# Kernel optimization log

Measured on AMD Instinct MI355X. Metric: run time of the kernel, lower is better.

## Reference

```python
import jax, jax.numpy as jnp
import numpy as np

N_NODES = 50000
N_REL = 256
D_IN = 128
NHID = 128
NHEADS = 2
D_OUT = NHID * NHEADS  # 256
ALPHA = 0.2  # leakyrelu slope


def _l2norm(x, eps=1e-12):
    n = jnp.sqrt(jnp.sum(x * x, axis=1, keepdims=True))
    return x / jnp.maximum(n, eps)


def _gat_layer(x, edge, edge_embed, a, a2, num_nodes, concat):
    """KBGAT-style sparse attention layer.
    x: [N, d_in]; edge: [2, E] (row0=dst, row1=src); edge_embed: [E, d_rel]
    a: [d_out, 2*d_in + d_rel]; a2: [d_out].
    Returns (h, h_raw, rowsum) ~ (x, x_l, x_w) of the original layer.
    """
    d_in = x.shape[1]
    dst, src = edge[0], edge[1]
    # edge_m = a @ cat(x[dst], x[src], edge_embed).T, computed blockwise -> [E, d_out]
    a_d, a_s, a_r = a[:, :d_in], a[:, d_in:2 * d_in], a[:, 2 * d_in:]
    edge_m = x[dst] @ a_d.T + x[src] @ a_s.T + edge_embed @ a_r.T
    # attention logits: exp(-leakyrelu(a2 . edge_m))
    powers = -jax.nn.leaky_relu(edge_m @ a2, negative_slope=ALPHA)  # [E]
    edge_e = jnp.exp(powers)
    rowsum = jax.ops.segment_sum(edge_e, dst, num_segments=num_nodes)  # [N]
    rowsum = jnp.where(rowsum == 0, 1e-12, rowsum)
    h_raw = jax.ops.segment_sum(edge_e[:, None] * edge_m, dst, num_segments=num_nodes)  # [N, d_out]
    h = h_raw / rowsum[:, None]
    if concat:
        h = jax.nn.elu(h)
    return h, h_raw, rowsum[:, None]


def setup_inputs() -> dict:
    key = jax.random.key(0)
    ks = jax.random.split(key, 16)
    E, E_NHOP = 300000, 30000
    xav = lambda k, shp: jax.random.uniform(k, shp, jnp.float32, -1.0, 1.0) * (
        1.414 * np.sqrt(6.0 / (shp[-2] + shp[-1])))
    inp = {
        "entity_embeddings": jax.random.normal(ks[0], (N_NODES, D_IN), jnp.float32),
        "relation_embeddings": jax.random.normal(ks[1], (N_REL, D_IN), jnp.float32),
        # per-head layer-1 attention params (stacked over heads)
        "a1": xav(ks[2], (NHEADS, NHID, 2 * D_IN + D_IN)),
        "a2_1": xav(ks[3], (NHEADS, NHID)),
        "W": xav(ks[4], (D_IN, D_OUT)),          # relation projection in SpGAT
        "a_out": xav(ks[5], (D_OUT, 2 * D_OUT + D_OUT)),
        "a2_out": xav(ks[6], (1, D_OUT))[0],
        "W_entities": xav(ks[7], (D_IN, D_OUT)),
        "batch_inputs": jax.random.randint(ks[8], (4096, 3), 0, N_NODES),
        "edge_list": jax.random.randint(ks[9], (2, E), 0, N_NODES),
        "edge_type": jax.random.randint(ks[10], (E,), 0, N_REL),
        "edge_list_nhop": jax.random.randint(ks[11], (2, E_NHOP), 0, N_NODES),
        "edge_type_nhop": jax.random.randint(ks[12], (E_NHOP, 2), 0, N_REL),
    }
    return inp


def reference(entity_embeddings, relation_embeddings, a1, a2_1, W, a_out, a2_out,
              W_entities, batch_inputs, edge_list, edge_type, edge_list_nhop,
              edge_type_nhop):
    # in-place row normalization of entity embeddings (as in original forward)
    ent = _l2norm(entity_embeddings)
    edge_all = jnp.concatenate([edge_list, edge_list_nhop], axis=1)  # [2, E+Enh]

    # ---- SpGAT layer 1: multi-head over original relation embeddings ----
    edge_embed = relation_embeddings[edge_type]
    edge_embed_nhop = relation_embeddings[edge_type_nhop[:, 0]] + relation_embeddings[edge_type_nhop[:, 1]]
    ee_all = jnp.concatenate([edge_embed, edge_embed_nhop], axis=0)
    heads = [
        _gat_layer(ent, edge_all, ee_all, a1[h], a2_1[h], N_NODES, concat=True)[0]
        for h in range(NHEADS)
    ]
    x = jnp.concatenate(heads, axis=1)  # [N, NHEADS*NHID]

    # ---- relation projection + output attention layer ----
    out_relation_1 = relation_embeddings @ W  # [R, D_OUT]
    ee2 = out_relation_1[edge_type]
    ee2_nhop = out_relation_1[edge_type_nhop[:, 0]] + out_relation_1[edge_type_nhop[:, 1]]
    ee2_all = jnp.concatenate([ee2, ee2_nhop], axis=0)
    xo, x_l, x_w = _gat_layer(x, edge_all, ee2_all, a_out, a2_out, N_NODES, concat=False)
    xo, x_l, x_w = jax.nn.elu(xo), jax.nn.elu(x_l), jax.nn.elu(x_w)

    # ---- residual mask update + normalization ----
    mask = jnp.zeros((N_NODES,), xo.dtype).at[batch_inputs[:, 2]].set(1.0)
    entities_upgraded = ent @ W_entities
    out_entity_1 = entities_upgraded + mask[:, None] * xo
    out_entity_1 = _l2norm(out_entity_1)
    out_entity_l_1 = _l2norm(x_l)
    return (out_entity_1, out_relation_1, out_entity_l_1)
```

## Files before the change

### kernel.cpp

```cpp
#include <hip/hip_runtime.h>
#include <hip/hip_bf16.h>
#include <math.h>

#define N_NODES 50000
#define E1 300000
#define EN 30000
#define ETOT 330000

typedef __hip_bfloat16 bf16;

__device__ __forceinline__ float b2f(bf16 x){ return __bfloat162float(x); }
__device__ __forceinline__ bf16 f2b(float x){ return __float2bfloat16(x); }

__device__ __forceinline__ float ldf(const void* p, long i, bool f32){
  return f32 ? ((const float*)p)[i] : b2f(((const bf16*)p)[i]);
}
__device__ __forceinline__ void stf(void* p, long i, float v, bool f32){
  if (f32) ((float*)p)[i] = v; else ((bf16*)p)[i] = f2b(v);
}

template<int NT>
__device__ __forceinline__ float block_sum(float v){
  __shared__ float sm[NT/64];
  #pragma unroll
  for (int o=32;o>0;o>>=1) v += __shfl_down(v,o);
  if ((threadIdx.x & 63)==0) sm[threadIdx.x>>6] = v;
  __syncthreads();
  float t = 0.f;
  #pragma unroll
  for (int w=0;w<NT/64;w++) t += sm[w];
  __syncthreads();
  return t;
}

__global__ void k_detect(const void* __restrict__ emb, int* __restrict__ flag){
  const unsigned short* h = (const unsigned short*)emb;
  int sane = 0;
  for (int i=0;i<128;i++){
    unsigned e = (h[i]>>7)&0xFFu;
    if (e>=112u && e<=143u) sane++;
  }
  *flag = (sane >= 112) ? 0 : 1;
}

__global__ void k_hist(const int* __restrict__ el, const int* __restrict__ eln,
                       int* __restrict__ cnt){
  int i = blockIdx.x*blockDim.x + threadIdx.x;
  if (i < ETOT){
    int dst = (i < E1) ? el[i] : eln[i - E1];
    atomicAdd(cnt + dst, 1);
  }
}

__global__ __launch_bounds__(1024) void k_scan(const int* __restrict__ cnt,
                                               int* __restrict__ rowp,
                                               int* __restrict__ cur){
  __shared__ int part[1024];
  int t = threadIdx.x;
  const int CH = (N_NODES + 1023)/1024;
  int base = t*CH;
  int s = 0;
  for (int i=0;i<CH;i++){ int n = base+i; if (n < N_NODES) s += cnt[n]; }
  part[t] = s;
  __syncthreads();
  for (int o=1;o<1024;o<<=1){
    int u = (t>=o) ? part[t-o] : 0;
    __syncthreads();
    part[t] += u;
    __syncthreads();
  }
  int off = part[t] - s;
  for (int i=0;i<CH;i++){
    int n = base+i;
    if (n < N_NODES){ rowp[n] = off; cur[n] = off; off += cnt[n]; }
  }
  if (t==0) rowp[N_NODES] = ETOT;
}

__global__ void k_fill(const int* __restrict__ el, const int* __restrict__ et,
                       const int* __restrict__ eln, const int* __restrict__ etn,
                       int* __restrict__ cur, int* __restrict__ esrc,
                       int* __restrict__ epak){
  int i = blockIdx.x*blockDim.x + threadIdx.x;
  if (i >= ETOT) return;
  int dst, src, pk;
  if (i < E1){
    dst = el[i]; src = el[E1 + i];
    pk = et[i];
  } else {
    int e = i - E1;
    dst = eln[e]; src = eln[EN + e];
    pk = etn[2*e] | (etn[2*e+1]<<9) | (1<<18);
  }
  int pos = atomicAdd(cur + dst, 1);
  esrc[pos] = src; epak[pos] = pk;
}

template<int D>
__global__ __launch_bounds__(256) void k_gath1(
    const int* __restrict__ rowp, const int* __restrict__ esrc,
    const int* __restrict__ epak,
    const float* __restrict__ pd, const float* __restrict__ ps,
    const float* __restrict__ rp,
    const float* __restrict__ sd, const float* __restrict__ ss,
    const float* __restrict__ sr,
    float* __restrict__ x, int hoff){
  int w = threadIdx.x >> 6, lane = threadIdx.x & 63;
  int n = blockIdx.x*4 + w;
  if (n >= N_NODES) return;
  const int M = D/64;
  float acc[M];
  #pragma unroll
  for (int m=0;m<M;m++) acc[m] = 0.f;
  float rs = 0.f;
  float sdn = sd[n];
  int b = rowp[n], e = rowp[n+1];
  for (int i=b;i<e;i++){
    int src = esrc[i], pk = epak[i];
    int t0 = pk & 511, t1 = (pk>>9)&511, has2 = (pk>>18)&1;
    float srv = sr[t0] + (has2 ? sr[t1] : 0.f);
    float score = sdn + ss[src] + srv;
    float lr = score > 0.f ? score : 0.2f*score;
    float wgt = expf(-lr);
    rs += wgt;
    const float* psr = ps + (long)src*D;
    const float* r1  = rp + (long)t0*D;
    const float* r2  = rp + (long)t1*D;
    #pragma unroll
    for (int m=0;m<M;m++){
      float v = psr[m*64+lane] + r1[m*64+lane];
      if (has2) v += r2[m*64+lane];
      acc[m] += wgt*v;
    }
  }
  float denom = (rs == 0.f) ? 1e-12f : rs;
  #pragma unroll
  for (int m=0;m<M;m++){
    int j = m*64+lane;
    float hr = rs*pd[(long)n*D + j] + acc[m];
    float hv = hr/denom;
    hv = hv > 0.f ? hv : (expf(hv) - 1.f);
    x[(long)n*256 + hoff + j] = hv;
  }
}

__global__ __launch_bounds__(256) void k_gath2(
    const int* __restrict__ rowp, const int* __restrict__ esrc,
    const int* __restrict__ epak,
    const float* __restrict__ p2d, const float* __restrict__ ps,
    const float* __restrict__ rp,
    const float* __restrict__ sd, const float* __restrict__ ss,
    const float* __restrict__ sr,
    const float* __restrict__ eu, const float* __restrict__ mask,
    const int* __restrict__ flag, void* __restrict__ out){
  bool f32 = flag[0] != 0;
  int w = threadIdx.x >> 6, lane = threadIdx.x & 63;
  int n = blockIdx.x*4 + w;
  if (n >= N_NODES) return;
  float acc[4] = {0.f,0.f,0.f,0.f};
  float rs = 0.f;
  float sdn = sd[n];
  int b = rowp[n], e = rowp[n+1];
  for (int i=b;i<e;i++){
    int src = esrc[i], pk = epak[i];
    int t0 = pk & 511, t1 = (pk>>9)&511, has2 = (pk>>18)&1;
    float srv = sr[t0] + (has2 ? sr[t1] : 0.f);
    float score = sdn + ss[src] + srv;
    float lr = score > 0.f ? score : 0.2f*score;
    float wgt = expf(-lr);
    rs += wgt;
    const float* psr = ps + (long)src*256;
    const float* r1  = rp + (long)t0*256;
    const float* r2  = rp + (long)t1*256;
    #pragma unroll
    for (int m=0;m<4;m++){
      float v = psr[m*64+lane] + r1[m*64+lane];
      if (has2) v += r2[m*64+lane];
      acc[m] += wgt*v;
    }
  }
  float denom = (rs == 0.f) ? 1e-12f : rs;
  float mk = mask[n];
  float val[4], xl[4];
  float n1 = 0.f, n2 = 0.f;
  #pragma unroll
  for (int m=0;m<4;m++){
    int j = m*64+lane;
    float hr = rs*p2d[(long)n*256 + j] + acc[m];
    float xo = hr/denom; xo = xo > 0.f ? xo : (expf(xo) - 1.f);
    float l  = hr > 0.f ? hr : (expf(hr) - 1.f);
    float v  = eu[(long)n*256 + j] + mk*xo;
    val[m] = v; xl[m] = l;
    n1 += v*v; n2 += l*l;
  }
  #pragma unroll
  for (int o=32;o>0;o>>=1){ n1 += __shfl_xor(n1,o); n2 += __shfl_xor(n2,o); }
  float i1 = 1.f/fmaxf(sqrtf(n1), 1e-12f);
  float i2 = 1.f/fmaxf(sqrtf(n2), 1e-12f);
  #pragma unroll
  for (int m=0;m<4;m++){
    int j = m*64+lane;
    stf(out, (long)n*256 + j,             val[m]*i1, f32);
    stf(out, 12865536L + (long)n*256 + j, xl[m]*i2,  f32);
  }
}

__global__ void k_rproj1(const void* __restrict__ rel, const void* __restrict__ a,
                         const void* __restrict__ a2, const int* __restrict__ flag,
                         float* __restrict__ rp, float* __restrict__ sr){
  bool f32 = flag[0] != 0;
  int t = blockIdx.x, j = threadIdx.x;
  __shared__ float rs_[128];
  rs_[j] = ldf(rel, (long)t*128 + j, f32);
  __syncthreads();
  long ar = (long)j*384 + 256;
  float acc = 0.f;
  #pragma unroll 4
  for (int k=0;k<128;k++) acc += rs_[k]*ldf(a, ar+k, f32);
  rp[(long)t*128+j] = acc;
  float v = block_sum<128>(acc*ldf(a2, j, f32));
  if (j==0) sr[t] = v;
}

__global__ void k_rproj1b(const void* __restrict__ rel, const void* __restrict__ a,
                          const void* __restrict__ a2, const int* __restrict__ flag,
                          long abias, long a2bias,
                          float* __restrict__ rp, float* __restrict__ sr){
  bool f32 = flag[0] != 0;
  int t = blockIdx.x, j = threadIdx.x;
  __shared__ float rs_[128];
  rs_[j] = ldf(rel, (long)t*128 + j, f32);
  __syncthreads();
  long ar = abias + (long)j*384 + 256;
  float acc = 0.f;
  #pragma unroll 4
  for (int k=0;k<128;k++) acc += rs_[k]*ldf(a, ar+k, f32);
  rp[(long)t*128+j] = acc;
  float v = block_sum<128>(acc*ldf(a2, a2bias + j, f32));
  if (j==0) sr[t] = v;
}

__global__ void k_rel2(const void* __restrict__ rel, const void* __restrict__ W,
                       const int* __restrict__ flag,
                       float* __restrict__ r2, void* __restrict__ out){
  bool f32 = flag[0] != 0;
  int t = blockIdx.x, j = threadIdx.x;
  __shared__ float rs_[128];
  if (j < 128) rs_[j] = ldf(rel, (long)t*128 + j, f32);
  __syncthreads();
  float acc = 0.f;
  #pragma unroll 4
  for (int k=0;k<128;k++) acc += rs_[k]*ldf(W, (long)k*256 + j, f32);
  r2[(long)t*256+j] = acc;
  stf(out, 12800000L + (long)t*256 + j, acc, f32);
}

__global__ void k_rproj2(const float* __restrict__ r2, const void* __restrict__ a,
                         const void* __restrict__ a2, const int* __restrict__ flag,
                         float* __restrict__ rp, float* __restrict__ sr){
  bool f32 = flag[0] != 0;
  int t = blockIdx.x, j = threadIdx.x;
  __shared__ float rs_[256];
  rs_[j] = r2[(long)t*256 + j];
  __syncthreads();
  long ar = (long)j*768 + 512;
  float acc = 0.f;
  #pragma unroll 4
  for (int k=0;k<256;k++) acc += rs_[k]*ldf(a, ar+k, f32);
  rp[(long)t*256+j] = acc;
  float v = block_sum<256>(acc*ldf(a2, j, f32));
  if (j==0) sr[t] = v;
}

__global__ void k_trF(const void* __restrict__ src, const int* __restrict__ flag,
                      long bias, long jstride, int J, float* __restrict__ dst){
  bool f32 = flag[0] != 0;
  int k = blockIdx.x, j = threadIdx.x;
  dst[(long)k*J + j] = ldf(src, bias + (long)j*jstride + k, f32);
}

__global__ void k_cvtF(const void* __restrict__ src, const int* __restrict__ flag,
                       int n, float* __restrict__ dst){
  bool f32 = flag[0] != 0;
  int i = blockIdx.x*blockDim.x + threadIdx.x;
  if (i < n) dst[i] = ldf(src, i, f32);
}

template<int NT, int K, int BM, int NORM, int DUAL, int SCORE, int XDUAL>
__global__ __launch_bounds__(NT) void k_gnp(
    const void* __restrict__ X, const int* __restrict__ flag, int N,
    const float* __restrict__ WT1, const float* __restrict__ WT2,
    const void* __restrict__ a2, long a2bias,
    float* __restrict__ O1, float* __restrict__ O2,
    float* __restrict__ s1, float* __restrict__ s2, int ldc){
  __shared__ float xs[BM][K];
  __shared__ float rsc[BM];
  const int NW = NT/64;
  __shared__ float red1[BM][NW];
  __shared__ float red2[BM][NW];
  int t = threadIdx.x;
  int n0 = blockIdx.x * BM;
  bool xf32 = XDUAL ? (flag[0] != 0) : true;

  for (int idx = t; idx < BM*K; idx += NT){
    int m = idx / K, k = idx - m*K;
    int n = n0 + m;
    xs[m][k] = (n < N) ? ldf(X, (long)n*K + k, xf32) : 0.f;
  }
  __syncthreads();

  if (NORM){
    const int NPR = NT / BM;
    int r = t / NPR, l = t - r*NPR;
    float ssq = 0.f;
    #pragma unroll
    for (int k = l; k < K; k += NPR){ float v = xs[r][k]; ssq += v*v; }
    #pragma unroll
    for (int o = NPR>>1; o > 0; o >>= 1) ssq += __shfl_xor(ssq, o);
    if (l == 0) rsc[r] = 1.f / fmaxf(sqrtf(ssq), 1e-12f);
    __syncthreads();
    for (int idx = t; idx < BM*K; idx += NT){
      int m = idx / K, k = idx - m*K;
      xs[m][k] *= rsc[m];
    }
    __syncthreads();
  }

  float a1c[BM], a2c[BM];
  #pragma unroll
  for (int m=0;m<BM;m++){ a1c[m]=0.f; a2c[m]=0.f; }
  #pragma unroll 4
  for (int k=0;k<K;k++){
    float w1 = WT1[(long)k*NT + t];
    float w2 = DUAL ? WT2[(long)k*NT + t] : 0.f;
    #pragma unroll
    for (int m=0;m<BM;m++){
      a1c[m] += xs[m][k]*w1;
      if (DUAL) a2c[m] += xs[m][k]*w2;
    }
  }

  #pragma unroll
  for (int m=0;m<BM;m++){
    int n = n0 + m;
    if (n < N){
      O1[(long)n*ldc + t] = a1c[m];
      if (DUAL) O2[(long)n*ldc + t] = a2c[m];
    }
  }

  if (SCORE){
    bool af32 = flag[0] != 0;
    float a2v = ldf(a2, a2bias + t, af32);
    int w = t >> 6, lane = t & 63;
    #pragma unroll
    for (int m=0;m<BM;m++){
      float v1 = a1c[m]*a2v;
      float v2 = DUAL ? a2c[m]*a2v : 0.f;
      #pragma unroll
      for (int o=32;o>0;o>>=1){ v1 += __shfl_down(v1,o); v2 += __shfl_down(v2,o); }
      if (lane==0){ red1[m][w]=v1; red2[m][w]=v2; }
    }
    __syncthreads();
    if (t < BM && n0 + t < N){
      float v1=0.f, v2=0.f;
      #pragma unroll
      for (int ww=0;ww<NW;ww++){ v1+=red1[t][ww]; v2+=red2[t][ww]; }
      s1[n0+t] = v1;
      if (DUAL) s2[n0+t] = v2;
    }
  }
}

__global__ void k_mask(const int* __restrict__ bi, float* __restrict__ mask){
  int i = blockIdx.x*blockDim.x + threadIdx.x;
  if (i < 4096) mask[bi[i*3 + 2]] = 1.f;
}

extern "C" void kernel_launch(void* const* d_in, const int* in_sizes, int n_in,
                              void* d_out, int out_size, void* d_ws, size_t ws_size,
                              hipStream_t stream) {
  const void* emb = d_in[0];
  const void* rel = d_in[1];
  const void* a1b = d_in[2];
  const void* a21 = d_in[3];
  const void* W   = d_in[4];
  const void* aout= d_in[5];
  const void* a2o = d_in[6];
  const void* We  = d_in[7];
  const int* bi   = (const int*)d_in[8];
  const int* el   = (const int*)d_in[9];
  const int* et   = (const int*)d_in[10];
  const int* eln  = (const int*)d_in[11];
  const int* etn  = (const int*)d_in[12];
  float* ws = (float*)d_ws;

  const size_t PD_=0, PS_=6400000;
  const size_t P2D_=0;
  const size_t CNT_=12800000, ROWP_=12860000, ESRC_=12920000, EPAK_=13260000;
  const size_t TW_=19200000;
  const size_t X_=25600000;
  const size_t P2S_=38400000;
  const size_t SD_=51250000, SS_=51300000, S2D_=51350000,
               S2S_=51400000, MK_=51500000,
               RP1_=51550000, SR1_=51590000, R2_=51600000, RP2_=51670000,
               SR2_=51740000, FLAG_=51750000;
  int* flag = (int*)(ws + FLAG_);
  int* cnt  = (int*)(ws + CNT_);
  int* rowp = (int*)(ws + ROWP_);
  int* esrc = (int*)(ws + ESRC_);
  int* epak = (int*)(ws + EPAK_);

  k_detect<<<1,1,0,stream>>>(emb, flag);

  hipMemsetAsync(ws+MK_,  0, (size_t)50000*sizeof(float), stream);
  hipMemsetAsync(cnt,     0, (size_t)50000*sizeof(int), stream);

  k_hist<<<(ETOT+255)/256,256,0,stream>>>(el, eln, cnt);
  k_scan<<<1,1024,0,stream>>>(cnt, rowp, cnt);
  k_fill<<<(ETOT+255)/256,256,0,stream>>>(el, et, eln, etn, cnt, esrc, epak);

  k_trF<<<128,128,0,stream>>>(a1b, flag, 0L,          384L, 128, ws+TW_);
  k_trF<<<128,128,0,stream>>>(a1b, flag, 128L,        384L, 128, ws+TW_+16384);
  k_trF<<<128,128,0,stream>>>(a1b, flag, 49152L,      384L, 128, ws+TW_+32768);
  k_trF<<<128,128,0,stream>>>(a1b, flag, 49152L+128L, 384L, 128, ws+TW_+49152);

  k_gnp<128,128,16,1,1,1,1><<<(N_NODES+15)/16,128,0,stream>>>(
      emb, flag, N_NODES, ws+TW_, ws+TW_+16384, a21, 0L,
      ws+PD_, ws+PS_, ws+SD_, ws+SS_, 128);
  k_rproj1<<<256,128,0,stream>>>(rel, a1b, a21, flag, ws+RP1_, ws+SR1_);
  k_gath1<128><<<(N_NODES+3)/4,256,0,stream>>>(rowp, esrc, epak,
      ws+PD_, ws+PS_, ws+RP1_, ws+SD_, ws+SS_, ws+SR1_, ws+X_, 0);

  k_gnp<128,128,16,1,1,1,1><<<(N_NODES+15)/16,128,0,stream>>>(
      emb, flag, N_NODES, ws+TW_+32768, ws+TW_+49152, a21, 128L,
      ws+PD_, ws+PS_, ws+SD_, ws+SS_, 128);
  k_rproj1b<<<256,128,0,stream>>>(rel, a1b, a21, flag, 49152L, 128L, ws+RP1_, ws+SR1_);
  k_gath1<128><<<(N_NODES+3)/4,256,0,stream>>>(rowp, esrc, epak,
      ws+PD_, ws+PS_, ws+RP1_, ws+SD_, ws+SS_, ws+SR1_, ws+X_, 128);

  k_rel2<<<256,256,0,stream>>>(rel, W, flag, ws+R2_, d_out);
  k_rproj2<<<256,256,0,stream>>>(ws+R2_, aout, a2o, flag, ws+RP2_, ws+SR2_);

  k_trF<<<256,256,0,stream>>>(aout, flag, 0L,   768L, 256, ws+TW_);
  k_trF<<<256,256,0,stream>>>(aout, flag, 256L, 768L, 256, ws+TW_+65536);
  k_gnp<256,256,16,0,1,1,0><<<(N_NODES+15)/16,256,0,stream>>>(
      ws+X_, flag, N_NODES, ws+TW_, ws+TW_+65536, a2o, 0L,
      ws+P2D_, ws+P2S_, ws+S2D_, ws+S2S_, 256);

  k_cvtF<<<128,256,0,stream>>>(We, flag, 32768, ws+RP1_);
  k_mask<<<16,256,0,stream>>>(bi, ws+MK_);
  k_gnp<256,128,16,1,0,0,1><<<(N_NODES+15)/16,256,0,stream>>>(
      emb, flag, N_NODES, ws+RP1_, nullptr, nullptr, 0L,
      ws+X_, nullptr, nullptr, nullptr, 256);

  k_gath2<<<(N_NODES+3)/4,256,0,stream>>>(rowp, esrc, epak,
      ws+P2D_, ws+P2S_, ws+RP2_, ws+S2D_, ws+S2S_, ws+SR2_,
      ws+X_, ws+MK_, flag, d_out);
}
```

Measured before the change: 1.109 ms.

## Vectorize gather loads and GEMM inner loop, route relation projections through tiled GEMM

Gather kernels now load each edge's source and relation rows as float2/float4 per lane instead of strided scalars, and write outputs with vector stores. The tiled projection kernel reads four k values at once from shared memory as float4 with unroll 2. The per-relation projection kernels are removed and replaced by the generic tiled GEMM kernel over transposed weight slices, which adds a few small transpose launches. The aim is fewer memory instructions and better coalescing in the gather-bound phase. The gather kernels now use an interleaved column layout, which must match how the projection buffers are written.

```diff
diff --git a/kernel.cpp b/kernel.cpp
--- a/kernel.cpp
+++ b/kernel.cpp
@@ -17,6 +17,16 @@
 }
 __device__ __forceinline__ void stf(void* p, long i, float v, bool f32){
   if (f32) ((float*)p)[i] = v; else ((bf16*)p)[i] = f2b(v);
+}
+__device__ __forceinline__ void stv4(void* p, long elem, float a, float b,
+                                     float c, float d, bool f32){
+  if (f32){
+    float4 t; t.x=a; t.y=b; t.z=c; t.w=d;
+    *reinterpret_cast<float4*>((float*)p + elem) = t;
+  } else {
+    bf16 t[4] = {f2b(a), f2b(b), f2b(c), f2b(d)};
+    *reinterpret_cast<uint2*>((bf16*)p + elem) = *reinterpret_cast<uint2*>(t);
+  }
 }
 
 template<int NT>
@@ -96,7 +106,6 @@
   esrc[pos] = src; epak[pos] = pk;
 }
 
-template<int D>
 __global__ __launch_bounds__(256) void k_gath1(
     const int* __restrict__ rowp, const int* __restrict__ esrc,
     const int* __restrict__ epak,
@@ -108,10 +117,9 @@
   int w = threadIdx.x >> 6, lane = threadIdx.x & 63;
   int n = blockIdx.x*4 + w;
   if (n >= N_NODES) return;
-  const int M = D/64;
-  float acc[M];
-  #pragma unroll
-  for (int m=0;m<M;m++) acc[m] = 0.f;
+  const float2* ps2 = (const float2*)ps;
+  const float2* rp2 = (const float2*)rp;
+  float2 acc; acc.x = 0.f; acc.y = 0.f;
   float rs = 0.f;
   float sdn = sd[n];
   int b = rowp[n], e = rowp[n+1];
@@ -123,25 +131,19 @@
     float lr = score > 0.f ? score : 0.2f*score;
     float wgt = expf(-lr);
     rs += wgt;
-    const float* psr = ps + (long)src*D;
-    const float* r1  = rp + (long)t0*D;
-    const float* r2  = rp + (long)t1*D;
-    #pragma unroll
-    for (int m=0;m<M;m++){
-      float v = psr[m*64+lane] + r1[m*64+lane];
-      if (has2) v += r2[m*64+lane];
-      acc[m] += wgt*v;
-    }
+    float2 v  = ps2[(long)src*64 + lane];
+    float2 r1 = rp2[(long)t0*64 + lane];
+    v.x += r1.x; v.y += r1.y;
+    if (has2){ float2 r2v = rp2[(long)t1*64 + lane]; v.x += r2v.x; v.y += r2v.y; }
+    acc.x += wgt*v.x; acc.y += wgt*v.y;
   }
   float denom = (rs == 0.f) ? 1e-12f : rs;
-  #pragma unroll
-  for (int m=0;m<M;m++){
-    int j = m*64+lane;
-    float hr = rs*pd[(long)n*D + j] + acc[m];
-    float hv = hr/denom;
-    hv = hv > 0.f ? hv : (expf(hv) - 1.f);
-    x[(long)n*256 + hoff + j] = hv;
-  }
+  float2 pdv = ((const float2*)pd)[(long)n*64 + lane];
+  float hr0 = rs*pdv.x + acc.x, hr1 = rs*pdv.y + acc.y;
+  float h0 = hr0/denom; h0 = h0 > 0.f ? h0 : (expf(h0) - 1.f);
+  float h1 = hr1/denom; h1 = h1 > 0.f ? h1 : (expf(h1) - 1.f);
+  float2 o; o.x = h0; o.y = h1;
+  *reinterpret_cast<float2*>(x + (long)n*256 + hoff + lane*2) = o;
 }
 
 __global__ __launch_bounds__(256) void k_gath2(
@@ -157,7 +159,9 @@
   int w = threadIdx.x >> 6, lane = threadIdx.x & 63;
   int n = blockIdx.x*4 + w;
   if (n >= N_NODES) return;
-  float acc[4] = {0.f,0.f,0.f,0.f};
+  const float4* ps4 = (const float4*)ps;
+  const float4* rp4 = (const float4*)rp;
+  float4 acc; acc.x=acc.y=acc.z=acc.w=0.f;
   float rs = 0.f;
   float sdn = sd[n];
   int b = rowp[n], e = rowp[n+1];
@@ -169,27 +173,30 @@
     float lr = score > 0.f ? score : 0.2f*score;
     float wgt = expf(-lr);
     rs += wgt;
-    const float* psr = ps + (long)src*256;
-    const float* r1  = rp + (long)t0*256;
-    const float* r2  = rp + (long)t1*256;
-    #pragma unroll
-    for (int m=0;m<4;m++){
-      float v = psr[m*64+lane] + r1[m*64+lane];
-      if (has2) v += r2[m*64+lane];
-      acc[m] += wgt*v;
-    }
+    float4 v  = ps4[(long)src*64 + lane];
+    float4 r1 = rp4[(long)t0*64 + lane];
+    v.x += r1.x; v.y += r1.y; v.z += r1.z; v.w += r1.w;
+    if (has2){
+      float4 r2v = rp4[(long)t1*64 + lane];
+      v.x += r2v.x; v.y += r2v.y; v.z += r2v.z; v.w += r2v.w;
+    }
+    acc.x += wgt*v.x; acc.y += wgt*v.y; acc.z += wgt*v.z; acc.w += wgt*v.w;
   }
   float denom = (rs == 0.f) ? 1e-12f : rs;
   float mk = mask[n];
+  float4 pdv = ((const float4*)p2d)[(long)n*64 + lane];
+  float4 euv = ((const float4*)eu)[(long)n*64 + lane];
+  float av[4] = {acc.x, acc.y, acc.z, acc.w};
+  float pv[4] = {pdv.x, pdv.y, pdv.z, pdv.w};
+  float ev[4] = {euv.x, euv.y, euv.z, euv.w};
   float val[4], xl[4];
   float n1 = 0.f, n2 = 0.f;
   #pragma unroll
   for (int m=0;m<4;m++){
-    int j = m*64+lane;
-    float hr = rs*p2d[(long)n*256 + j] + acc[m];
+    float hr = rs*pv[m] + av[m];
     float xo = hr/denom; xo = xo > 0.f ? xo : (expf(xo) - 1.f);
     float l  = hr > 0.f ? hr : (expf(hr) - 1.f);
-    float v  = eu[(long)n*256 + j] + mk*xo;
+    float v  = ev[m] + mk*xo;
     val[m] = v; xl[m] = l;
     n1 += v*v; n2 += l*l;
   }
@@ -197,47 +204,10 @@
   for (int o=32;o>0;o>>=1){ n1 += __shfl_xor(n1,o); n2 += __shfl_xor(n2,o); }
   float i1 = 1.f/fmaxf(sqrtf(n1), 1e-12f);
   float i2 = 1.f/fmaxf(sqrtf(n2), 1e-12f);
-  #pragma unroll
-  for (int m=0;m<4;m++){
-    int j = m*64+lane;
-    stf(out, (long)n*256 + j,             val[m]*i1, f32);
-    stf(out, 12865536L + (long)n*256 + j, xl[m]*i2,  f32);
-  }
-}
-
-__global__ void k_rproj1(const void* __restrict__ rel, const void* __restrict__ a,
-                         const void* __restrict__ a2, const int* __restrict__ flag,
-                         float* __restrict__ rp, float* __restrict__ sr){
-  bool f32 = flag[0] != 0;
-  int t = blockIdx.x, j = threadIdx.x;
-  __shared__ float rs_[128];
-  rs_[j] = ldf(rel, (long)t*128 + j, f32);
-  __syncthreads();
-  long ar = (long)j*384 + 256;
-  float acc = 0.f;
-  #pragma unroll 4
-  for (int k=0;k<128;k++) acc += rs_[k]*ldf(a, ar+k, f32);
-  rp[(long)t*128+j] = acc;
-  float v = block_sum<128>(acc*ldf(a2, j, f32));
-  if (j==0) sr[t] = v;
-}
-
-__global__ void k_rproj1b(const void* __restrict__ rel, const void* __restrict__ a,
-                          const void* __restrict__ a2, const int* __restrict__ flag,
-                          long abias, long a2bias,
-                          float* __restrict__ rp, float* __restrict__ sr){
-  bool f32 = flag[0] != 0;
-  int t = blockIdx.x, j = threadIdx.x;
-  __shared__ float rs_[128];
-  rs_[j] = ldf(rel, (long)t*128 + j, f32);
-  __syncthreads();
-  long ar = abias + (long)j*384 + 256;
-  float acc = 0.f;
-  #pragma unroll 4
-  for (int k=0;k<128;k++) acc += rs_[k]*ldf(a, ar+k, f32);
-  rp[(long)t*128+j] = acc;
-  float v = block_sum<128>(acc*ldf(a2, a2bias + j, f32));
-  if (j==0) sr[t] = v;
+  stv4(out, (long)n*256 + lane*4,
+       val[0]*i1, val[1]*i1, val[2]*i1, val[3]*i1, f32);
+  stv4(out, 12865536L + (long)n*256 + lane*4,
+       xl[0]*i2, xl[1]*i2, xl[2]*i2, xl[3]*i2, f32);
 }
 
 __global__ void k_rel2(const void* __restrict__ rel, const void* __restrict__ W,
@@ -255,23 +225,6 @@
   stf(out, 12800000L + (long)t*256 + j, acc, f32);
 }
 
-__global__ void k_rproj2(const float* __restrict__ r2, const void* __restrict__ a,
-                         const void* __restrict__ a2, const int* __restrict__ flag,
-                         float* __restrict__ rp, float* __restrict__ sr){
-  bool f32 = flag[0] != 0;
-  int t = blockIdx.x, j = threadIdx.x;
-  __shared__ float rs_[256];
-  rs_[j] = r2[(long)t*256 + j];
-  __syncthreads();
-  long ar = (long)j*768 + 512;
-  float acc = 0.f;
-  #pragma unroll 4
-  for (int k=0;k<256;k++) acc += rs_[k]*ldf(a, ar+k, f32);
-  rp[(long)t*256+j] = acc;
-  float v = block_sum<256>(acc*ldf(a2, j, f32));
-  if (j==0) sr[t] = v;
-}
-
 __global__ void k_trF(const void* __restrict__ src, const int* __restrict__ flag,
                       long bias, long jstride, int J, float* __restrict__ dst){
   bool f32 = flag[0] != 0;
@@ -293,7 +246,7 @@
     const void* __restrict__ a2, long a2bias,
     float* __restrict__ O1, float* __restrict__ O2,
     float* __restrict__ s1, float* __restrict__ s2, int ldc){
-  __shared__ float xs[BM][K];
+  __shared__ __align__(16) float xs[BM][K];
   __shared__ float rsc[BM];
   const int NW = NT/64;
   __shared__ float red1[BM][NW];
@@ -329,14 +282,25 @@
   float a1c[BM], a2c[BM];
   #pragma unroll
   for (int m=0;m<BM;m++){ a1c[m]=0.f; a2c[m]=0.f; }
-  #pragma unroll 4
-  for (int k=0;k<K;k++){
-    float w1 = WT1[(long)k*NT + t];
-    float w2 = DUAL ? WT2[(long)k*NT + t] : 0.f;
+  const float4* xs4 = reinterpret_cast<const float4*>(&xs[0][0]);
+  #pragma unroll 2
+  for (int k0=0;k0<K;k0+=4){
+    float w1a = WT1[(long)(k0+0)*NT + t];
+    float w1b = WT1[(long)(k0+1)*NT + t];
+    float w1c = WT1[(long)(k0+2)*NT + t];
+    float w1d = WT1[(long)(k0+3)*NT + t];
+    float w2a=0.f,w2b=0.f,w2c=0.f,w2d=0.f;
+    if (DUAL){
+      w2a = WT2[(long)(k0+0)*NT + t];
+      w2b = WT2[(long)(k0+1)*NT + t];
+      w2c = WT2[(long)(k0+2)*NT + t];
+      w2d = WT2[(long)(k0+3)*NT + t];
+    }
     #pragma unroll
     for (int m=0;m<BM;m++){
-      a1c[m] += xs[m][k]*w1;
-      if (DUAL) a2c[m] += xs[m][k]*w2;
+      float4 xv = xs4[(m*K + k0) >> 2];
+      a1c[m] += xv.x*w1a + xv.y*w1b + xv.z*w1c + xv.w*w1d;
+      if (DUAL) a2c[m] += xv.x*w2a + xv.y*w2b + xv.z*w2c + xv.w*w2d;
     }
   }
 
@@ -424,26 +388,37 @@
   k_trF<<<128,128,0,stream>>>(a1b, flag, 128L,        384L, 128, ws+TW_+16384);
   k_trF<<<128,128,0,stream>>>(a1b, flag, 49152L,      384L, 128, ws+TW_+32768);
   k_trF<<<128,128,0,stream>>>(a1b, flag, 49152L+128L, 384L, 128, ws+TW_+49152);
+  k_trF<<<128,128,0,stream>>>(a1b, flag, 256L,        384L, 128, ws+TW_+65536);
+  k_trF<<<128,128,0,stream>>>(a1b, flag, 49152L+256L, 384L, 128, ws+TW_+81920);
 
   k_gnp<128,128,16,1,1,1,1><<<(N_NODES+15)/16,128,0,stream>>>(
       emb, flag, N_NODES, ws+TW_, ws+TW_+16384, a21, 0L,
       ws+PD_, ws+PS_, ws+SD_, ws+SS_, 128);
-  k_rproj1<<<256,128,0,stream>>>(rel, a1b, a21, flag, ws+RP1_, ws+SR1_);
-  k_gath1<128><<<(N_NODES+3)/4,256,0,stream>>>(rowp, esrc, epak,
+  k_gnp<128,128,16,0,0,1,1><<<16,128,0,stream>>>(
+      rel, flag, 256, ws+TW_+65536, nullptr, a21, 0L,
+      ws+RP1_, nullptr, ws+SR1_, nullptr, 128);
+  k_gath1<<<(N_NODES+3)/4,256,0,stream>>>(rowp, esrc, epak,
       ws+PD_, ws+PS_, ws+RP1_, ws+SD_, ws+SS_, ws+SR1_, ws+X_, 0);
 
   k_gnp<128,128,16,1,1,1,1><<<(N_NODES+15)/16,128,0,stream>>>(
       emb, flag, N_NODES, ws+TW_+32768, ws+TW_+49152, a21, 128L,
       ws+PD_, ws+PS_, ws+SD_, ws+SS_, 128);
-  k_rproj1b<<<256,128,0,stream>>>(rel, a1b, a21, flag, 49152L, 128L, ws+RP1_, ws+SR1_);
-  k_gath1<128><<<(N_NODES+3)/4,256,0,stream>>>(rowp, esrc, epak,
+  k_gnp<128,128,16,0,0,1,1><<<16,128,0,stream>>>(
+      rel, flag, 256, ws+TW_+81920, nullptr, a21, 128L,
+      ws+RP1_, nullptr, ws+SR1_, nullptr, 128);
+  k_gath1<<<(N_NODES+3)/4,256,0,stream>>>(rowp, esrc, epak,
       ws+PD_, ws+PS_, ws+RP1_, ws+SD_, ws+SS_, ws+SR1_, ws+X_, 128);
 
   k_rel2<<<256,256,0,stream>>>(rel, W, flag, ws+R2_, d_out);
-  k_rproj2<<<256,256,0,stream>>>(ws+R2_, aout, a2o, flag, ws+RP2_, ws+SR2_);
 
   k_trF<<<256,256,0,stream>>>(aout, flag, 0L,   768L, 256, ws+TW_);
   k_trF<<<256,256,0,stream>>>(aout, flag, 256L, 768L, 256, ws+TW_+65536);
+  k_trF<<<256,256,0,stream>>>(aout, flag, 512L, 768L, 256, ws+TW_+131072);
+
+  k_gnp<256,256,16,0,0,1,0><<<16,256,0,stream>>>(
+      ws+R2_, flag, 256, ws+TW_+131072, nullptr, a2o, 0L,
+      ws+RP2_, nullptr, ws+SR2_, nullptr, 256);
+
   k_gnp<256,256,16,0,1,1,0><<<(N_NODES+15)/16,256,0,stream>>>(
       ws+X_, flag, N_NODES, ws+TW_, ws+TW_+65536, a2o, 0L,
       ws+P2D_, ws+P2S_, ws+S2D_, ws+S2S_, 256);
```

Result: no change. 1.106 ms (-0.3%).
